# Performance work log

Hardware: AMD Instinct MI355X
Metric: run time of the kernel (lower is better)

## Reference

```python
import jax, jax.numpy as jnp
import numpy as np

B, C, H, W = 16, 16, 96, 320


def _hat(phi):
    z = jnp.zeros_like(phi[..., 0])
    px, py, pz = phi[..., 0], phi[..., 1], phi[..., 2]
    return jnp.stack([
        jnp.stack([z, -pz, py], -1),
        jnp.stack([pz, z, -px], -1),
        jnp.stack([-py, px, z], -1)], -2)


def se3_exp(xi):
    # xi: [B,6] twist (rho, phi) -> [B,4,4] SE3 matrix
    rho, phi = xi[:, :3], xi[:, 3:6]
    th2 = jnp.sum(phi * phi, -1)
    small = th2 < 1e-8
    th2s = jnp.where(small, 1.0, th2)
    th = jnp.sqrt(th2s)
    A = jnp.where(small, 1.0 - th2 / 6.0, jnp.sin(th) / th)
    Bc = jnp.where(small, 0.5 - th2 / 24.0, (1.0 - jnp.cos(th)) / th2s)
    Cc = jnp.where(small, 1.0 / 6.0 - th2 / 120.0, (th - jnp.sin(th)) / (th2s * th))
    K = _hat(phi)
    K2 = K @ K
    I = jnp.eye(3, dtype=xi.dtype)
    R = I + A[:, None, None] * K + Bc[:, None, None] * K2
    V = I + Bc[:, None, None] * K + Cc[:, None, None] * K2
    t = V @ rho[..., None]
    top = jnp.concatenate([R, t], -1)
    bot = jnp.broadcast_to(jnp.array([0.0, 0.0, 0.0, 1.0], xi.dtype), (xi.shape[0], 1, 4))
    return jnp.concatenate([top, bot], 1)


def grid_sample(im, grid):
    # torch F.grid_sample: bilinear, padding_mode='zeros', align_corners=False
    Bb, Cc, Hh, Ww = im.shape
    x = (grid[..., 0] + 1.0) * (Ww * 0.5) - 0.5
    y = (grid[..., 1] + 1.0) * (Hh * 0.5) - 0.5
    x0 = jnp.floor(x); y0 = jnp.floor(y)
    wx = x - x0; wy = y - y0
    x0i = x0.astype(jnp.int32); y0i = y0.astype(jnp.int32)

    def one(imb, x0b, y0b, wxb, wyb):
        def g(ix, iy):
            valid = ((ix >= 0) & (ix < Ww) & (iy >= 0) & (iy < Hh)).astype(imb.dtype)
            v = imb[:, jnp.clip(iy, 0, Hh - 1), jnp.clip(ix, 0, Ww - 1)]
            return v * valid[None]
        v00 = g(x0b, y0b); v01 = g(x0b + 1, y0b)
        v10 = g(x0b, y0b + 1); v11 = g(x0b + 1, y0b + 1)
        wxb = wxb[None]; wyb = wyb[None]
        return (v00 * (1 - wxb) * (1 - wyb) + v01 * wxb * (1 - wyb)
                + v10 * (1 - wxb) * wyb + v11 * wxb * wyb)

    return jax.vmap(one)(im, x0i, y0i, wx, wy)


def setup_inputs():
    key = jax.random.key(0)
    ks = jax.random.split(key, 10)
    # projected pixel coords (center) + 4 finite-difference taps
    xc = jax.random.uniform(ks[0], (B, H, W), jnp.float32, 2.0, W - 3.0)
    yc = jax.random.uniform(ks[1], (B, H, W), jnp.float32, 2.0, H - 3.0)
    xs = jnp.stack([xc, xc + 1, xc - 1, xc, xc], 1)
    ys = jnp.stack([yc, yc, yc, yc + 1, yc - 1], 1)
    p2 = jnp.stack([xs, ys], 1)[:, :, None]  # [B,2,1,5,H,W]
    XY = jax.random.normal(ks[2], (B, 2, H * W)) * 2.0
    Z = 1.0 + 10.0 * jax.random.uniform(ks[3], (B, 1, H * W))
    P2 = jnp.concatenate([XY, Z], 1)  # [B,3,HW], Z > 0
    f = 250.0 + 50.0 * jax.random.uniform(ks[4], (B,))
    K = jnp.zeros((B, 3, 3)).at[:, 0, 0].set(f).at[:, 1, 1].set(f)
    K = K.at[:, 0, 2].set(W / 2).at[:, 1, 2].set(H / 2).at[:, 2, 2].set(1.0)
    poses = se3_exp(0.1 * jax.random.normal(ks[5], (B, 6)))
    return dict(
        poses=poses, calib_K=K, p2=p2, P2=P2,
        weight=jax.random.uniform(ks[6], (B, 1, H, W), jnp.float32, 0.2, 1.0),
        src_feat=jax.random.normal(ks[7], (B, C, H, W)),
        tgt_feat=jax.random.normal(ks[8], (B, C, H, W)),
        src_w=jax.random.uniform(ks[9], (B, 1, H, W), jnp.float32, 0.3, 1.0),
        tgt_w=jax.random.uniform(jax.random.fold_in(key, 11), (B, 1, H, W), jnp.float32, 0.3, 1.0),
    )


def reference(poses, calib_K, p2, P2, weight, src_feat, tgt_feat, src_w, tgt_w):
    Bb, Cc, Hh, Ww = src_feat.shape
    HW = Hh * Ww
    # --- sample_tgt ---
    grid_pix = p2.transpose(2, 0, 4, 5, 3, 1).reshape(Bb, HW, 5, 2)  # n1 == 1
    gx = 2 * (grid_pix[..., :1] + 0.5) / Ww - 1
    gy = 2 * (grid_pix[..., 1:] + 0.5) / Hh - 1
    grid = jnp.concatenate([gx, gy], -1)  # [B,HW,5,2]
    f = grid_sample(tgt_feat, grid).reshape(Bb, Cc, Hh, Ww, 5)
    warped_tgt_feat = f[..., 0]
    grads = jnp.stack([(f[..., 1] - f[..., 2]) * 0.5,
                       (f[..., 3] - f[..., 4]) * 0.5], -1)  # [B,C,H,W,2]
    warped_tgt_w = grid_sample(tgt_w, grid[:, :, :1]).reshape(Bb, 1, Hh, Ww)
    # --- per-pixel 2x6 pixel->pose Jacobian ---
    X, Y, Z = P2[:, 0], P2[:, 1], P2[:, 2]  # [B,HW]
    fx = calib_K[:, 0, 0][:, None]; fy = calib_K[:, 1, 1][:, None]
    fxZ = fx / Z; fyZ = fy / Z
    fxXZ2 = fxZ * X / Z; fyYZ2 = fyZ * Y / Z
    zeros = jnp.zeros_like(fxXZ2)
    row0 = jnp.stack([fxZ, zeros, -fxXZ2, -fxXZ2 * Y, fx + fxXZ2 * X, -fxZ * Y], 1)
    row1 = jnp.stack([zeros, fyZ, -fyYZ2, -fy - fyYZ2 * Y, fyYZ2 * X, fyZ * X], 1)
    J_pixel_xi = jnp.stack([row0, row1], 1).transpose(0, 3, 1, 2)  # [B,HW,2,6]
    J_img_pixel = grads.reshape(Bb, Cc, HW, 2).transpose(0, 2, 1, 3)  # [B,HW,C,2]
    J = -(J_img_pixel @ J_pixel_xi)  # [B,HW,C,6]
    res = (src_feat - warped_tgt_feat).transpose(0, 2, 3, 1).reshape(Bb, HW, Cc)
    w = (src_w * warped_tgt_w * weight).reshape(Bb, HW)
    JW = J * w[:, :, None, None]
    Hm = jnp.einsum('bpck,bpcl->bkl', JW, J)  # [B,6,6] Gauss-Newton Hessian
    b = -jnp.einsum('bpc,bpck->bk', res, JW)  # [B,6]
    # H is SPD (sum of w*J^T J, w>0): solve == cholesky_solve of the original
    update = jnp.linalg.solve(Hm, b[..., None])[..., 0]  # [B,6]
    new_poses = se3_exp(update) @ poses
    return new_poses, update
```

## Files before the change

### kernel.cpp

```cpp
#include <hip/hip_runtime.h>
#include <math.h>

#define BATCH 16
#define CHN   16
#define IMH   96
#define IMW   320
#define HW    (IMH*IMW)
#define PPB   128
#define NBLK  (HW/PPB)
#define NPART 27
#define TWB   (HW*4)
#define RECB  (HW*16)

typedef __attribute__((ext_vector_type(2))) float f32x2;

__device__ __forceinline__ float dpp_row_sum(float x) {
    union fi { float f; int i; };
    fi v; v.f = x;
#define DPPSTEP(CTRL) { fi t; t.i = __builtin_amdgcn_update_dpp(0, v.i, CTRL, 0xf, 0xf, true); v.f += t.f; }
    DPPSTEP(0x111)
    DPPSTEP(0x112)
    DPPSTEP(0x114)
    DPPSTEP(0x118)
#undef DPPSTEP
    return v.f;
}

__global__ __launch_bounds__(256) void build_maps(const float* __restrict__ in,
                                                  const float* __restrict__ tw,
                                                  char* __restrict__ rec,
                                                  char* __restrict__ twr) {
    const int b = blockIdx.y;
    const int p = blockIdx.x * 256 + threadIdx.x;
    const int y = p / IMW, x = p - y * IMW;
    const float* ip = in + (size_t)b * CHN * HW + p;
    float f[16];
#pragma unroll
    for (int c = 0; c < 16; ++c) f[c] = ip[c * HW];

    unsigned d0 = 0, d1 = 0;
    d0 = __builtin_amdgcn_cvt_scalef32_pk_fp4_f32(d0, f[0],  f[1],  1.0f, 0);
    d0 = __builtin_amdgcn_cvt_scalef32_pk_fp4_f32(d0, f[2],  f[3],  1.0f, 1);
    d0 = __builtin_amdgcn_cvt_scalef32_pk_fp4_f32(d0, f[4],  f[5],  1.0f, 2);
    d0 = __builtin_amdgcn_cvt_scalef32_pk_fp4_f32(d0, f[6],  f[7],  1.0f, 3);
    d1 = __builtin_amdgcn_cvt_scalef32_pk_fp4_f32(d1, f[8],  f[9],  1.0f, 0);
    d1 = __builtin_amdgcn_cvt_scalef32_pk_fp4_f32(d1, f[10], f[11], 1.0f, 1);
    d1 = __builtin_amdgcn_cvt_scalef32_pk_fp4_f32(d1, f[12], f[13], 1.0f, 2);
    d1 = __builtin_amdgcn_cvt_scalef32_pk_fp4_f32(d1, f[14], f[15], 1.0f, 3);

    int* rb = (int*)(rec + (size_t)b * RECB);
    const int self = p * 4;
    rb[self + 0] = (int)d0;
    rb[self + 2] = (int)d1;
    if (y > 0) {
        const int up = (p - IMW) * 4;
        rb[up + 1] = (int)d0;
        rb[up + 3] = (int)d1;
    }
    if (y == IMH - 1) {
        rb[self + 1] = (int)d0;
        rb[self + 3] = (int)d1;
    }

    const float* twb = tw + (size_t)b * HW;
    const int xp1 = min(x + 1, IMW - 1), yp1 = min(y + 1, IMH - 1);
    const float v00 = twb[p];
    const float v01 = twb[y * IMW + xp1];
    const float v10 = twb[yp1 * IMW + x];
    const float v11 = twb[yp1 * IMW + xp1];
    int wq = __builtin_amdgcn_cvt_pk_fp8_f32(v00, v01, 0, false);
    wq     = __builtin_amdgcn_cvt_pk_fp8_f32(v10, v11, wq, true);
    ((int*)(twr + (size_t)b * TWB))[p] = wq;
}

__global__ __launch_bounds__(256, 2) void gn_accum(
    const float* __restrict__ p2,
    const float* __restrict__ P2,
    const float* __restrict__ calibK,
    const float* __restrict__ weight,
    const float* __restrict__ src_feat,
    const float* __restrict__ src_w,
    const char* __restrict__ twr,
    const char* __restrict__ rec,
    float* __restrict__ partials)
{
    __shared__ float xs_l[768];
    __shared__ float ys_l[768];
    __shared__ float red[16][NPART];

    const int n   = blockIdx.x;
    const int b   = n & 15;
    const int blk = n >> 4;
    const int t   = threadIdx.x;
    const int m   = t >> 1;
    const int h   = t & 1;
    const int pp  = blk * PPB + m;

    const unsigned Gblk0 = ((unsigned)b * HW + (unsigned)(blk * PPB)) * 5u;
#pragma unroll
    for (int j = 0; j < 3; ++j) {
        const unsigned idx = (unsigned)(j * 256 + t);
        if (idx < 640) {
            const unsigned G    = Gblk0 + idx;
            const unsigned sBig = G / (unsigned)(BATCH * HW);
            const unsigned r    = G - sBig * (unsigned)(BATCH * HW);
            const unsigned bb   = r / (unsigned)HW;
            const unsigned q    = r - bb * (unsigned)HW;
            const float* pb = p2 + (size_t)bb * (10 * HW) + (size_t)sBig * HW + q;
            xs_l[idx] = pb[0];
            ys_l[idx] = pb[5 * HW];
        }
    }
    __syncthreads();

    float wxs[5], wys[5];
    int   off[5];
    int   twoff = 0;
#pragma unroll
    for (int s = 0; s < 5; ++s) {
        const float xp = xs_l[5 * m + s];
        const float yp = ys_l[5 * m + s];
        float gx = 2.0f * (xp + 0.5f) / (float)IMW - 1.0f;
        float gy = 2.0f * (yp + 0.5f) / (float)IMH - 1.0f;
        float x  = (gx + 1.0f) * ((float)IMW * 0.5f) - 0.5f;
        float y  = (gy + 1.0f) * ((float)IMH * 0.5f) - 0.5f;
        float x0 = floorf(x), y0 = floorf(y);
        wxs[s] = x - x0;
        wys[s] = y - y0;
        int xi = (int)x0, yi = (int)y0;
        xi = min(max(xi, 0), IMW - 2);
        yi = min(max(yi, 0), IMH - 2);
        off[s] = (yi * IMW + xi) * 16;
        if (s == 0) twoff = (yi * IMW + xi) * 4;
    }

    const char* mapb = rec + (size_t)b * RECB + h * 8;
    int2 L0[5], L1[5];
#pragma unroll
    for (int s = 0; s < 5; ++s) {
        L0[s] = *(const int2*)(mapb + off[s]);
        L1[s] = *(const int2*)(mapb + off[s] + 16);
    }
    const int twq = *(const int*)(twr + (size_t)b * TWB + twoff);

    float srcv[8];
    const float* srcb = src_feat + (size_t)b * CHN * HW + (size_t)h * 8 * HW + pp;
#pragma unroll
    for (int j = 0; j < 8; ++j) srcv[j] = srcb[j * HW];

    const float* P2b = P2 + (size_t)b * 3 * HW;
    const float X = P2b[pp], Y = P2b[HW + pp], Z = P2b[2 * HW + pp];
    const float wP  = weight[(size_t)b * HW + pp];
    const float swP = src_w[(size_t)b * HW + pp];

    const float fx = calibK[b * 9 + 0];
    const float fy = calibK[b * 9 + 4];
    const float fxZ = fx / Z, fyZ = fy / Z;
    const float fxXZ2 = fxZ * X / Z;
    const float fyYZ2 = fyZ * Y / Z;
    float r0[6] = { fxZ, 0.0f, -fxXZ2, -fxXZ2 * Y, fx + fxXZ2 * X, -fxZ * Y };
    float r1[6] = { 0.0f, fyZ, -fyYZ2, -fy - fyYZ2 * Y, fyYZ2 * X, fyZ * X };

    float w00[5], w01[5], w10[5], w11[5];
#pragma unroll
    for (int s = 0; s < 5; ++s) {
        float wx = wxs[s], wy = wys[s];
        w00[s] = (1.0f - wx) * (1.0f - wy);
        w01[s] = wx * (1.0f - wy);
        w10[s] = (1.0f - wx) * wy;
        w11[s] = wx * wy;
    }

    float wtw;
    {
        const float wx = wxs[0], wy = wys[0];
        f32x2 wlo = __builtin_amdgcn_cvt_pk_f32_fp8(twq, false);
        f32x2 whi = __builtin_amdgcn_cvt_pk_f32_fp8(twq, true);
        wtw = wlo[0] * (1.0f - wx) * (1.0f - wy) + wlo[1] * wx * (1.0f - wy)
            + whi[0] * (1.0f - wx) * wy          + whi[1] * wx * wy;
    }
    const float w = swP * wtw * wP;

    f32x2 SxxV = {0.f,0.f}, SxyV = {0.f,0.f}, SyyV = {0.f,0.f}, TxV = {0.f,0.f}, TyV = {0.f,0.f};
#define PAIRSTEP(K) {                                                             \
        f32x2 fsv[5];                                                             \
        _Pragma("unroll")                                                         \
        for (int s = 0; s < 5; ++s) {                                             \
            fsv[s] = __builtin_amdgcn_cvt_scalef32_pk_f32_fp4(L0[s].x, 1.0f, K) * w00[s] \
                   + __builtin_amdgcn_cvt_scalef32_pk_f32_fp4(L1[s].x, 1.0f, K) * w01[s] \
                   + __builtin_amdgcn_cvt_scalef32_pk_f32_fp4(L0[s].y, 1.0f, K) * w10[s] \
                   + __builtin_amdgcn_cvt_scalef32_pk_f32_fp4(L1[s].y, 1.0f, K) * w11[s]; \
        }                                                                         \
        const f32x2 sr = { srcv[2 * (K)], srcv[2 * (K) + 1] };                    \
        f32x2 resv = sr - fsv[0];                                                 \
        f32x2 gxv  = (fsv[1] - fsv[2]) * 0.5f;                                    \
        f32x2 gyv  = (fsv[3] - fsv[4]) * 0.5f;                                    \
        SxxV += gxv * gxv; SxyV += gxv * gyv; SyyV += gyv * gyv;                  \
        TxV  += resv * gxv; TyV += resv * gyv; }
    PAIRSTEP(0) PAIRSTEP(1) PAIRSTEP(2) PAIRSTEP(3)
#undef PAIRSTEP

    const float Sxx = SxxV[0] + SxxV[1];
    const float Sxy = SxyV[0] + SxyV[1];
    const float Syy = SyyV[0] + SyyV[1];
    const float Tx  = TxV[0]  + TxV[1];
    const float Ty  = TyV[0]  + TyV[1];

    const float Pm = w * Sxx, Qm = w * Sxy, Rm = w * Syy;
    const float tx = w * Tx,  ty = w * Ty;

    float av[6], cv[6];
#pragma unroll
    for (int k = 0; k < 6; ++k) {
        av[k] = Pm * r0[k] + Qm * r1[k];
        cv[k] = Qm * r0[k] + Rm * r1[k];
    }

    const int wv   = t >> 6;
    const int lane = t & 63;
    const int rrow = (wv << 2) | (lane >> 4);
    const bool wr  = (lane & 15) == 15;

    int idx = 0;
#pragma unroll
    for (int k = 0; k < 6; ++k) {
#pragma unroll
        for (int l = 0; l < 6; ++l) {
            if (l < k) continue;
            float v = r0[k] * av[l] + r1[k] * cv[l];
            v = dpp_row_sum(v);
            if (wr) red[rrow][idx] = v;
            ++idx;
        }
    }
#pragma unroll
    for (int k = 0; k < 6; ++k) {
        float v = tx * r0[k] + ty * r1[k];
        v = dpp_row_sum(v);
        if (wr) red[rrow][21 + k] = v;
    }
    __syncthreads();
    if (t < NPART) {
        float s = 0.0f;
#pragma unroll
        for (int r = 0; r < 16; ++r) s += red[r][t];
        partials[((size_t)b * NBLK + blk) * NPART + t] = s;
    }
}

__global__ __launch_bounds__(256) void gn_solve(
    const float* __restrict__ partials,
    const float* __restrict__ poses,
    float* __restrict__ out)
{
    const int b = blockIdx.x;
    const int t = threadIdx.x;
    __shared__ double dsum[8][NPART];
    __shared__ double sums[NPART];

    if (t < 216) {
        const int col = t % NPART;
        const int g   = t / NPART;
        double s = 0.0;
        for (int j = g; j < NBLK; j += 8)
            s += (double)partials[((size_t)b * NBLK + j) * NPART + col];
        dsum[g][col] = s;
    }
    __syncthreads();
    if (t < NPART) {
        double s = 0.0;
#pragma unroll
        for (int g = 0; g < 8; ++g) s += dsum[g][t];
        sums[t] = s;
    }
    __syncthreads();
    if (t != 0) return;

    double A[6][7];
    {
        int idx = 0;
        for (int k = 0; k < 6; ++k)
            for (int l = k; l < 6; ++l) {
                A[k][l] = sums[idx];
                A[l][k] = sums[idx];
                ++idx;
            }
        for (int k = 0; k < 6; ++k) A[k][6] = sums[21 + k];
    }
    for (int col = 0; col < 6; ++col) {
        int piv = col; double mx = fabs(A[col][col]);
        for (int rr = col + 1; rr < 6; ++rr) {
            double v = fabs(A[rr][col]);
            if (v > mx) { mx = v; piv = rr; }
        }
        if (piv != col)
            for (int j = col; j < 7; ++j) { double tmp = A[col][j]; A[col][j] = A[piv][j]; A[piv][j] = tmp; }
        double d = A[col][col];
        for (int rr = col + 1; rr < 6; ++rr) {
            double f = A[rr][col] / d;
            for (int j = col; j < 7; ++j) A[rr][j] -= f * A[col][j];
        }
    }
    double x[6];
    for (int i = 5; i >= 0; --i) {
        double s = A[i][6];
        for (int j = i + 1; j < 6; ++j) s -= A[i][j] * x[j];
        x[i] = s / A[i][i];
    }

    const double rho[3] = { x[0], x[1], x[2] };
    const double phi[3] = { x[3], x[4], x[5] };
    const double th2 = phi[0]*phi[0] + phi[1]*phi[1] + phi[2]*phi[2];
    const bool small = th2 < 1e-8;
    const double th2s = small ? 1.0 : th2;
    const double th = sqrt(th2s);
    const double Ac = small ? 1.0 - th2 / 6.0   : sin(th) / th;
    const double Bc = small ? 0.5 - th2 / 24.0  : (1.0 - cos(th)) / th2s;
    const double Cc = small ? 1.0/6.0 - th2/120.0 : (th - sin(th)) / (th2s * th);
    const double Kh[3][3] = { { 0.0, -phi[2],  phi[1] },
                              {  phi[2], 0.0, -phi[0] },
                              { -phi[1],  phi[0], 0.0 } };
    double K2[3][3];
    for (int i = 0; i < 3; ++i)
        for (int j = 0; j < 3; ++j) {
            double s = 0.0;
            for (int k = 0; k < 3; ++k) s += Kh[i][k] * Kh[k][j];
            K2[i][j] = s;
        }
    double T[4][4];
    for (int i = 0; i < 3; ++i)
        for (int j = 0; j < 3; ++j) {
            double I = (i == j) ? 1.0 : 0.0;
            T[i][j] = I + Ac * Kh[i][j] + Bc * K2[i][j];
        }
    for (int i = 0; i < 3; ++i) {
        double s = 0.0;
        for (int j = 0; j < 3; ++j) {
            double I = (i == j) ? 1.0 : 0.0;
            double V = I + Bc * Kh[i][j] + Cc * K2[i][j];
            s += V * rho[j];
        }
        T[i][3] = s;
    }
    T[3][0] = 0.0; T[3][1] = 0.0; T[3][2] = 0.0; T[3][3] = 1.0;

    const float* pz = poses + b * 16;
    for (int i = 0; i < 4; ++i)
        for (int j = 0; j < 4; ++j) {
            double s = 0.0;
            for (int k = 0; k < 4; ++k) s += T[i][k] * (double)pz[k * 4 + j];
            out[b * 16 + i * 4 + j] = (float)s;
        }
    for (int k = 0; k < 6; ++k)
        out[BATCH * 16 + b * 6 + k] = (float)x[k];
}

extern "C" void kernel_launch(void* const* d_in, const int* in_sizes, int n_in,
                              void* d_out, int out_size, void* d_ws, size_t ws_size,
                              hipStream_t stream) {
    const float* poses    = (const float*)d_in[0];
    const float* calibK   = (const float*)d_in[1];
    const float* p2       = (const float*)d_in[2];
    const float* P2       = (const float*)d_in[3];
    const float* weight   = (const float*)d_in[4];
    const float* src_feat = (const float*)d_in[5];
    const float* tgt_feat = (const float*)d_in[6];
    const float* src_w    = (const float*)d_in[7];
    const float* tgt_w    = (const float*)d_in[8];
    float* out = (float*)d_out;

    char*  rec      = (char*)d_ws;
    char*  twr      = rec + (size_t)BATCH * RECB;
    float* partials = (float*)(twr + (size_t)BATCH * TWB);

    hipLaunchKernelGGL(build_maps, dim3(HW / 256, BATCH), dim3(256), 0, stream,
                       tgt_feat, tgt_w, rec, twr);
    hipLaunchKernelGGL(gn_accum, dim3(NBLK * BATCH), dim3(256), 0, stream,
                       p2, P2, calibK, weight, src_feat, src_w, twr, rec, partials);
    hipLaunchKernelGGL(gn_solve, dim3(BATCH), dim3(256), 0, stream,
                       partials, poses, out);
}
```

Before: 55.00 us.

## Map one pixel per thread with 64-thread blocks and transpose partials layout

```diff
diff --git a/kernel.cpp b/kernel.cpp
--- a/kernel.cpp
+++ b/kernel.cpp
@@ -6,8 +6,8 @@
 #define IMH   96
 #define IMW   320
 #define HW    (IMH*IMW)
-#define PPB   128
-#define NBLK  (HW/PPB)
+#define PPB   64
+#define NSLOT (HW/PPB)
 #define NPART 27
 #define TWB   (HW*4)
 #define RECB  (HW*16)
@@ -47,20 +47,11 @@
     d1 = __builtin_amdgcn_cvt_scalef32_pk_fp4_f32(d1, f[10], f[11], 1.0f, 1);
     d1 = __builtin_amdgcn_cvt_scalef32_pk_fp4_f32(d1, f[12], f[13], 1.0f, 2);
     d1 = __builtin_amdgcn_cvt_scalef32_pk_fp4_f32(d1, f[14], f[15], 1.0f, 3);
-
-    int* rb = (int*)(rec + (size_t)b * RECB);
-    const int self = p * 4;
-    rb[self + 0] = (int)d0;
-    rb[self + 2] = (int)d1;
-    if (y > 0) {
-        const int up = (p - IMW) * 4;
-        rb[up + 1] = (int)d0;
-        rb[up + 3] = (int)d1;
-    }
-    if (y == IMH - 1) {
-        rb[self + 1] = (int)d0;
-        rb[self + 3] = (int)d1;
-    }
+    int2 lv; lv.x = (int)d0; lv.y = (int)d1;
+    char* rb = rec + (size_t)b * RECB;
+    *(int2*)(rb + (size_t)p * 16) = lv;
+    if (y > 0)        *(int2*)(rb + (size_t)(p - IMW) * 16 + 8) = lv;
+    if (y == IMH - 1) *(int2*)(rb + (size_t)p * 16 + 8) = lv;
 
     const float* twb = tw + (size_t)b * HW;
     const int xp1 = min(x + 1, IMW - 1), yp1 = min(y + 1, IMH - 1);
@@ -73,7 +64,7 @@
     ((int*)(twr + (size_t)b * TWB))[p] = wq;
 }
 
-__global__ __launch_bounds__(256, 2) void gn_accum(
+__global__ __launch_bounds__(64, 4) void gn_accum(
     const float* __restrict__ p2,
     const float* __restrict__ P2,
     const float* __restrict__ calibK,
@@ -84,32 +75,28 @@
     const char* __restrict__ rec,
     float* __restrict__ partials)
 {
-    __shared__ float xs_l[768];
-    __shared__ float ys_l[768];
-    __shared__ float red[16][NPART];
+    __shared__ float xs_l[320];
+    __shared__ float ys_l[320];
+    __shared__ float red[4][NPART];
 
     const int n   = blockIdx.x;
     const int b   = n & 15;
     const int blk = n >> 4;
     const int t   = threadIdx.x;
-    const int m   = t >> 1;
-    const int h   = t & 1;
-    const int pp  = blk * PPB + m;
+    const int p   = blk * PPB + t;
 
     const unsigned Gblk0 = ((unsigned)b * HW + (unsigned)(blk * PPB)) * 5u;
 #pragma unroll
-    for (int j = 0; j < 3; ++j) {
-        const unsigned idx = (unsigned)(j * 256 + t);
-        if (idx < 640) {
-            const unsigned G    = Gblk0 + idx;
-            const unsigned sBig = G / (unsigned)(BATCH * HW);
-            const unsigned r    = G - sBig * (unsigned)(BATCH * HW);
-            const unsigned bb   = r / (unsigned)HW;
-            const unsigned q    = r - bb * (unsigned)HW;
-            const float* pb = p2 + (size_t)bb * (10 * HW) + (size_t)sBig * HW + q;
-            xs_l[idx] = pb[0];
-            ys_l[idx] = pb[5 * HW];
-        }
+    for (int j = 0; j < 5; ++j) {
+        const unsigned idx  = (unsigned)(j * 64 + t);
+        const unsigned G    = Gblk0 + idx;
+        const unsigned sBig = G / (unsigned)(BATCH * HW);
+        const unsigned r    = G - sBig * (unsigned)(BATCH * HW);
+        const unsigned bb   = r / (unsigned)HW;
+        const unsigned q    = r - bb * (unsigned)HW;
+        const float* pb = p2 + (size_t)bb * (10 * HW) + (size_t)sBig * HW + q;
+        xs_l[idx] = pb[0];
+        ys_l[idx] = pb[5 * HW];
     }
     __syncthreads();
 
@@ -118,8 +105,8 @@
     int   twoff = 0;
 #pragma unroll
     for (int s = 0; s < 5; ++s) {
-        const float xp = xs_l[5 * m + s];
-        const float yp = ys_l[5 * m + s];
+        const float xp = xs_l[5 * t + s];
+        const float yp = ys_l[5 * t + s];
         float gx = 2.0f * (xp + 0.5f) / (float)IMW - 1.0f;
         float gy = 2.0f * (yp + 0.5f) / (float)IMH - 1.0f;
         float x  = (gx + 1.0f) * ((float)IMW * 0.5f) - 0.5f;
@@ -134,24 +121,24 @@
         if (s == 0) twoff = (yi * IMW + xi) * 4;
     }
 
-    const char* mapb = rec + (size_t)b * RECB + h * 8;
-    int2 L0[5], L1[5];
+    const char* mapb = rec + (size_t)b * RECB;
+    int4 L0[5], L1[5];
 #pragma unroll
     for (int s = 0; s < 5; ++s) {
-        L0[s] = *(const int2*)(mapb + off[s]);
-        L1[s] = *(const int2*)(mapb + off[s] + 16);
+        L0[s] = *(const int4*)(mapb + off[s]);
+        L1[s] = *(const int4*)(mapb + off[s] + 16);
     }
     const int twq = *(const int*)(twr + (size_t)b * TWB + twoff);
 
-    float srcv[8];
-    const float* srcb = src_feat + (size_t)b * CHN * HW + (size_t)h * 8 * HW + pp;
-#pragma unroll
-    for (int j = 0; j < 8; ++j) srcv[j] = srcb[j * HW];
+    float srcv[16];
+    const float* srcb = src_feat + (size_t)b * CHN * HW + p;
+#pragma unroll
+    for (int c = 0; c < 16; ++c) srcv[c] = srcb[c * HW];
 
     const float* P2b = P2 + (size_t)b * 3 * HW;
-    const float X = P2b[pp], Y = P2b[HW + pp], Z = P2b[2 * HW + pp];
-    const float wP  = weight[(size_t)b * HW + pp];
-    const float swP = src_w[(size_t)b * HW + pp];
+    const float X = P2b[p], Y = P2b[HW + p], Z = P2b[2 * HW + p];
+    const float wP  = weight[(size_t)b * HW + p];
+    const float swP = src_w[(size_t)b * HW + p];
 
     const float fx = calibK[b * 9 + 0];
     const float fy = calibK[b * 9 + 4];
@@ -182,22 +169,27 @@
     const float w = swP * wtw * wP;
 
     f32x2 SxxV = {0.f,0.f}, SxyV = {0.f,0.f}, SyyV = {0.f,0.f}, TxV = {0.f,0.f}, TyV = {0.f,0.f};
-#define PAIRSTEP(K) {                                                             \
+#define PAIRSTEP(H, K) {                                                          \
         f32x2 fsv[5];                                                             \
         _Pragma("unroll")                                                         \
         for (int s = 0; s < 5; ++s) {                                             \
-            fsv[s] = __builtin_amdgcn_cvt_scalef32_pk_f32_fp4(L0[s].x, 1.0f, K) * w00[s] \
-                   + __builtin_amdgcn_cvt_scalef32_pk_f32_fp4(L1[s].x, 1.0f, K) * w01[s] \
-                   + __builtin_amdgcn_cvt_scalef32_pk_f32_fp4(L0[s].y, 1.0f, K) * w10[s] \
-                   + __builtin_amdgcn_cvt_scalef32_pk_f32_fp4(L1[s].y, 1.0f, K) * w11[s]; \
+            const int ad = (H) ? L0[s].y : L0[s].x;                               \
+            const int bd = (H) ? L1[s].y : L1[s].x;                               \
+            const int cd = (H) ? L0[s].w : L0[s].z;                               \
+            const int dd = (H) ? L1[s].w : L1[s].z;                               \
+            fsv[s] = __builtin_amdgcn_cvt_scalef32_pk_f32_fp4(ad, 1.0f, K) * w00[s] \
+                   + __builtin_amdgcn_cvt_scalef32_pk_f32_fp4(bd, 1.0f, K) * w01[s] \
+                   + __builtin_amdgcn_cvt_scalef32_pk_f32_fp4(cd, 1.0f, K) * w10[s] \
+                   + __builtin_amdgcn_cvt_scalef32_pk_f32_fp4(dd, 1.0f, K) * w11[s]; \
         }                                                                         \
-        const f32x2 sr = { srcv[2 * (K)], srcv[2 * (K) + 1] };                    \
+        const f32x2 sr = { srcv[(H) * 8 + 2 * (K)], srcv[(H) * 8 + 2 * (K) + 1] };\
         f32x2 resv = sr - fsv[0];                                                 \
         f32x2 gxv  = (fsv[1] - fsv[2]) * 0.5f;                                    \
         f32x2 gyv  = (fsv[3] - fsv[4]) * 0.5f;                                    \
         SxxV += gxv * gxv; SxyV += gxv * gyv; SyyV += gyv * gyv;                  \
         TxV  += resv * gxv; TyV += resv * gyv; }
-    PAIRSTEP(0) PAIRSTEP(1) PAIRSTEP(2) PAIRSTEP(3)
+    PAIRSTEP(0, 0) PAIRSTEP(0, 1) PAIRSTEP(0, 2) PAIRSTEP(0, 3)
+    PAIRSTEP(1, 0) PAIRSTEP(1, 1) PAIRSTEP(1, 2) PAIRSTEP(1, 3)
 #undef PAIRSTEP
 
     const float Sxx = SxxV[0] + SxxV[1];
@@ -216,10 +208,8 @@
         cv[k] = Qm * r0[k] + Rm * r1[k];
     }
 
-    const int wv   = t >> 6;
-    const int lane = t & 63;
-    const int rrow = (wv << 2) | (lane >> 4);
-    const bool wr  = (lane & 15) == 15;
+    const int rrow = t >> 4;
+    const bool wr  = (t & 15) == 15;
 
     int idx = 0;
 #pragma unroll
@@ -241,10 +231,8 @@
     }
     __syncthreads();
     if (t < NPART) {
-        float s = 0.0f;
-#pragma unroll
-        for (int r = 0; r < 16; ++r) s += red[r][t];
-        partials[((size_t)b * NBLK + blk) * NPART + t] = s;
+        float s = red[0][t] + red[1][t] + red[2][t] + red[3][t];
+        partials[((size_t)b * NPART + t) * NSLOT + blk] = s;
     }
 }
 
@@ -261,9 +249,10 @@
     if (t < 216) {
         const int col = t % NPART;
         const int g   = t / NPART;
+        const float* pb = partials + ((size_t)b * NPART + col) * NSLOT;
         double s = 0.0;
-        for (int j = g; j < NBLK; j += 8)
-            s += (double)partials[((size_t)b * NBLK + j) * NPART + col];
+        for (int j = g; j < NSLOT; j += 8)
+            s += (double)pb[j];
         dsum[g][col] = s;
     }
     __syncthreads();
@@ -375,7 +364,7 @@
 
     hipLaunchKernelGGL(build_maps, dim3(HW / 256, BATCH), dim3(256), 0, stream,
                        tgt_feat, tgt_w, rec, twr);
-    hipLaunchKernelGGL(gn_accum, dim3(NBLK * BATCH), dim3(256), 0, stream,
+    hipLaunchKernelGGL(gn_accum, dim3(NSLOT * BATCH), dim3(PPB), 0, stream,
                        p2, P2, calibK, weight, src_feat, src_w, twr, rec, partials);
     hipLaunchKernelGGL(gn_solve, dim3(BATCH), dim3(256), 0, stream,
                        partials, poses, out);
```

Measured after the change: 53.39 us. -2.9%, faster.

## Split sample taps across thread pairs instead of channels, exchange gradients via DPP

Applied to the files above, without the earlier changes.

```diff
diff --git a/kernel.cpp b/kernel.cpp
--- a/kernel.cpp
+++ b/kernel.cpp
@@ -26,6 +26,13 @@
     return v.f;
 }
 
+__device__ __forceinline__ float dpp_swap_pair(float x) {
+    union fi { float f; int i; };
+    fi v; v.f = x;
+    v.i = __builtin_amdgcn_update_dpp(0, v.i, 0xB1, 0xf, 0xf, true);
+    return v.f;
+}
+
 __global__ __launch_bounds__(256) void build_maps(const float* __restrict__ in,
                                                   const float* __restrict__ tw,
                                                   char* __restrict__ rec,
@@ -47,20 +54,11 @@
     d1 = __builtin_amdgcn_cvt_scalef32_pk_fp4_f32(d1, f[10], f[11], 1.0f, 1);
     d1 = __builtin_amdgcn_cvt_scalef32_pk_fp4_f32(d1, f[12], f[13], 1.0f, 2);
     d1 = __builtin_amdgcn_cvt_scalef32_pk_fp4_f32(d1, f[14], f[15], 1.0f, 3);
-
-    int* rb = (int*)(rec + (size_t)b * RECB);
-    const int self = p * 4;
-    rb[self + 0] = (int)d0;
-    rb[self + 2] = (int)d1;
-    if (y > 0) {
-        const int up = (p - IMW) * 4;
-        rb[up + 1] = (int)d0;
-        rb[up + 3] = (int)d1;
-    }
-    if (y == IMH - 1) {
-        rb[self + 1] = (int)d0;
-        rb[self + 3] = (int)d1;
-    }
+    int2 lv; lv.x = (int)d0; lv.y = (int)d1;
+    char* rb = rec + (size_t)b * RECB;
+    *(int2*)(rb + (size_t)p * 16) = lv;
+    if (y > 0)        *(int2*)(rb + (size_t)(p - IMW) * 16 + 8) = lv;
+    if (y == IMH - 1) *(int2*)(rb + (size_t)p * 16 + 8) = lv;
 
     const float* twb = tw + (size_t)b * HW;
     const int xp1 = min(x + 1, IMW - 1), yp1 = min(y + 1, IMH - 1);
@@ -73,7 +71,7 @@
     ((int*)(twr + (size_t)b * TWB))[p] = wq;
 }
 
-__global__ __launch_bounds__(256, 2) void gn_accum(
+__global__ __launch_bounds__(256, 6) void gn_accum(
     const float* __restrict__ p2,
     const float* __restrict__ P2,
     const float* __restrict__ calibK,
@@ -84,8 +82,8 @@
     const char* __restrict__ rec,
     float* __restrict__ partials)
 {
-    __shared__ float xs_l[768];
-    __shared__ float ys_l[768];
+    __shared__ float xs_l[640];
+    __shared__ float ys_l[640];
     __shared__ float red[16][NPART];
 
     const int n   = blockIdx.x;
@@ -113,11 +111,13 @@
     }
     __syncthreads();
 
-    float wxs[5], wys[5];
-    int   off[5];
+    float wx0s = 0.f, wy0s = 0.f;
     int   twoff = 0;
-#pragma unroll
-    for (int s = 0; s < 5; ++s) {
+    int   o[3];
+    float W[3][4];
+#pragma unroll
+    for (int ls = 0; ls < 3; ++ls) {
+        const int s = h ? ((ls == 0) ? 3 : (ls == 1) ? 4 : 0) : ls;
         const float xp = xs_l[5 * m + s];
         const float yp = ys_l[5 * m + s];
         float gx = 2.0f * (xp + 0.5f) / (float)IMW - 1.0f;
@@ -125,33 +125,76 @@
         float x  = (gx + 1.0f) * ((float)IMW * 0.5f) - 0.5f;
         float y  = (gy + 1.0f) * ((float)IMH * 0.5f) - 0.5f;
         float x0 = floorf(x), y0 = floorf(y);
-        wxs[s] = x - x0;
-        wys[s] = y - y0;
+        float wx = x - x0, wy = y - y0;
         int xi = (int)x0, yi = (int)y0;
         xi = min(max(xi, 0), IMW - 2);
         yi = min(max(yi, 0), IMH - 2);
-        off[s] = (yi * IMW + xi) * 16;
-        if (s == 0) twoff = (yi * IMW + xi) * 4;
-    }
-
-    const char* mapb = rec + (size_t)b * RECB + h * 8;
-    int2 L0[5], L1[5];
-#pragma unroll
-    for (int s = 0; s < 5; ++s) {
-        L0[s] = *(const int2*)(mapb + off[s]);
-        L1[s] = *(const int2*)(mapb + off[s] + 16);
+        o[ls] = (yi * IMW + xi) * 16;
+        W[ls][0] = (1.0f - wx) * (1.0f - wy);
+        W[ls][1] = wx * (1.0f - wy);
+        W[ls][2] = (1.0f - wx) * wy;
+        W[ls][3] = wx * wy;
+        if (s == 0) { twoff = (yi * IMW + xi) * 4; wx0s = wx; wy0s = wy; }
+    }
+
+    const char* mapb = rec + (size_t)b * RECB;
+    int4 g0 = *(const int4*)(mapb + o[0]);
+    int4 g1 = *(const int4*)(mapb + o[0] + 16);
+    int4 g2 = *(const int4*)(mapb + o[1]);
+    int4 g3 = *(const int4*)(mapb + o[1] + 16);
+    int4 g4 = g0, g5 = g1;
+    if (h == 0) {
+        g4 = *(const int4*)(mapb + o[2]);
+        g5 = *(const int4*)(mapb + o[2] + 16);
     }
     const int twq = *(const int*)(twr + (size_t)b * TWB + twoff);
-
-    float srcv[8];
-    const float* srcb = src_feat + (size_t)b * CHN * HW + (size_t)h * 8 * HW + pp;
-#pragma unroll
-    for (int j = 0; j < 8; ++j) srcv[j] = srcb[j * HW];
-
+    float srcv[16];
+    const float* srcb = src_feat + (size_t)b * CHN * HW + pp;
+#pragma unroll
+    for (int c = 0; c < 16; ++c) srcv[c] = srcb[c * HW];
     const float* P2b = P2 + (size_t)b * 3 * HW;
     const float X = P2b[pp], Y = P2b[HW + pp], Z = P2b[2 * HW + pp];
     const float wP  = weight[(size_t)b * HW + pp];
     const float swP = src_w[(size_t)b * HW + pp];
+
+    float wtw;
+    {
+        f32x2 wlo = __builtin_amdgcn_cvt_pk_f32_fp8(twq, false);
+        f32x2 whi = __builtin_amdgcn_cvt_pk_f32_fp8(twq, true);
+        wtw = wlo[0] * (1.0f - wx0s) * (1.0f - wy0s) + wlo[1] * wx0s * (1.0f - wy0s)
+            + whi[0] * (1.0f - wx0s) * wy0s          + whi[1] * wx0s * wy0s;
+    }
+    const float w = swP * wtw * wP;
+
+    f32x2 SxxV = {0.f,0.f}, SxyV = {0.f,0.f}, SyyV = {0.f,0.f}, TxV = {0.f,0.f}, TyV = {0.f,0.f};
+#define MIX(GA, GB, WQ, H, K) ( \
+      __builtin_amdgcn_cvt_scalef32_pk_f32_fp4((H) ? GA.y : GA.x, 1.0f, K) * WQ[0] \
+    + __builtin_amdgcn_cvt_scalef32_pk_f32_fp4((H) ? GB.y : GB.x, 1.0f, K) * WQ[1] \
+    + __builtin_amdgcn_cvt_scalef32_pk_f32_fp4((H) ? GA.w : GA.z, 1.0f, K) * WQ[2] \
+    + __builtin_amdgcn_cvt_scalef32_pk_f32_fp4((H) ? GB.w : GB.z, 1.0f, K) * WQ[3] )
+#define PAIRSTEP(H, K) {                                                          \
+        f32x2 a0 = MIX(g0, g1, W[0], H, K);                                       \
+        f32x2 a1 = MIX(g2, g3, W[1], H, K);                                       \
+        f32x2 a2 = MIX(g4, g5, W[2], H, K);                                       \
+        f32x2 snd = (a0 - a1) * 0.5f;                   \
+        f32x2 gyv;                                                                \
+        gyv[0] = dpp_swap_pair(snd[0]);                                           \
+        gyv[1] = dpp_swap_pair(snd[1]);                                           \
+        const f32x2 sr = { srcv[(H) * 8 + 2 * (K)], srcv[(H) * 8 + 2 * (K) + 1] };\
+        f32x2 resv = sr - a0;                                 \
+        f32x2 gxv  = (a1 - a2) * 0.5f;                       \
+        SxxV += gxv * gxv; SxyV += gxv * gyv; SyyV += gyv * gyv;                  \
+        TxV  += resv * gxv; TyV += resv * gyv; }
+    PAIRSTEP(0, 0) PAIRSTEP(0, 1) PAIRSTEP(0, 2) PAIRSTEP(0, 3)
+    PAIRSTEP(1, 0) PAIRSTEP(1, 1) PAIRSTEP(1, 2) PAIRSTEP(1, 3)
+#undef PAIRSTEP
+#undef MIX
+
+    const float Sxx = h ? 0.0f : (SxxV[0] + SxxV[1]);
+    const float Sxy = h ? 0.0f : (SxyV[0] + SxyV[1]);
+    const float Syy = h ? 0.0f : (SyyV[0] + SyyV[1]);
+    const float Tx  = h ? 0.0f : (TxV[0]  + TxV[1]);
+    const float Ty  = h ? 0.0f : (TyV[0]  + TyV[1]);
 
     const float fx = calibK[b * 9 + 0];
     const float fy = calibK[b * 9 + 4];
@@ -160,51 +203,6 @@
     const float fyYZ2 = fyZ * Y / Z;
     float r0[6] = { fxZ, 0.0f, -fxXZ2, -fxXZ2 * Y, fx + fxXZ2 * X, -fxZ * Y };
     float r1[6] = { 0.0f, fyZ, -fyYZ2, -fy - fyYZ2 * Y, fyYZ2 * X, fyZ * X };
-
-    float w00[5], w01[5], w10[5], w11[5];
-#pragma unroll
-    for (int s = 0; s < 5; ++s) {
-        float wx = wxs[s], wy = wys[s];
-        w00[s] = (1.0f - wx) * (1.0f - wy);
-        w01[s] = wx * (1.0f - wy);
-        w10[s] = (1.0f - wx) * wy;
-        w11[s] = wx * wy;
-    }
-
-    float wtw;
-    {
-        const float wx = wxs[0], wy = wys[0];
-        f32x2 wlo = __builtin_amdgcn_cvt_pk_f32_fp8(twq, false);
-        f32x2 whi = __builtin_amdgcn_cvt_pk_f32_fp8(twq, true);
-        wtw = wlo[0] * (1.0f - wx) * (1.0f - wy) + wlo[1] * wx * (1.0f - wy)
-            + whi[0] * (1.0f - wx) * wy          + whi[1] * wx * wy;
-    }
-    const float w = swP * wtw * wP;
-
-    f32x2 SxxV = {0.f,0.f}, SxyV = {0.f,0.f}, SyyV = {0.f,0.f}, TxV = {0.f,0.f}, TyV = {0.f,0.f};
-#define PAIRSTEP(K) {                                                             \
-        f32x2 fsv[5];                                                             \
-        _Pragma("unroll")                                                         \
-        for (int s = 0; s < 5; ++s) {                                             \
-            fsv[s] = __builtin_amdgcn_cvt_scalef32_pk_f32_fp4(L0[s].x, 1.0f, K) * w00[s] \
-                   + __builtin_amdgcn_cvt_scalef32_pk_f32_fp4(L1[s].x, 1.0f, K) * w01[s] \
-                   + __builtin_amdgcn_cvt_scalef32_pk_f32_fp4(L0[s].y, 1.0f, K) * w10[s] \
-                   + __builtin_amdgcn_cvt_scalef32_pk_f32_fp4(L1[s].y, 1.0f, K) * w11[s]; \
-        }                                                                         \
-        const f32x2 sr = { srcv[2 * (K)], srcv[2 * (K) + 1] };                    \
-        f32x2 resv = sr - fsv[0];                                                 \
-        f32x2 gxv  = (fsv[1] - fsv[2]) * 0.5f;                                    \
-        f32x2 gyv  = (fsv[3] - fsv[4]) * 0.5f;                                    \
-        SxxV += gxv * gxv; SxyV += gxv * gyv; SyyV += gyv * gyv;                  \
-        TxV  += resv * gxv; TyV += resv * gyv; }
-    PAIRSTEP(0) PAIRSTEP(1) PAIRSTEP(2) PAIRSTEP(3)
-#undef PAIRSTEP
-
-    const float Sxx = SxxV[0] + SxxV[1];
-    const float Sxy = SxyV[0] + SxyV[1];
-    const float Syy = SyyV[0] + SyyV[1];
-    const float Tx  = TxV[0]  + TxV[1];
-    const float Ty  = TyV[0]  + TyV[1];
 
     const float Pm = w * Sxx, Qm = w * Sxy, Rm = w * Syy;
     const float tx = w * Tx,  ty = w * Ty;
```

Result: slower. 70.45 us (+28.1%).
